# Optimization experiments

Hardware: AMD Instinct MI355X
Metric: run time of the kernel (lower is better)

Reference implementation:

```python
import jax, jax.numpy as jnp
import numpy as np

V = 50257      # vocab size
H = 512        # hidden size
S = 128        # source length
BEAM = 5       # beam width (matches beam_width=5 default)
TMAX = 32      # MAX_LENGTH decode cap
SOS, EOS = 1, 2
NEG = -1e9


def setup_inputs() -> dict:
    key = jax.random.key(0)
    ks = jax.random.split(key, 12)
    p = lambda k, shape: jax.random.normal(k, shape, jnp.float32) * 0.02
    return {
        "input_tokens": jax.random.randint(ks[0], (S,), 0, V),
        "embedding": p(ks[1], (V, H)),
        "enc_Wih": p(ks[2], (3 * H, H)),
        "enc_Whh": p(ks[3], (3 * H, H)),
        "enc_bih": jnp.zeros((3 * H,), jnp.float32),
        "enc_bhh": jnp.zeros((3 * H,), jnp.float32),
        "dec_Wih": p(ks[4], (3 * H, H)),
        "dec_Whh": p(ks[5], (3 * H, H)),
        "dec_bih": jnp.zeros((3 * H,), jnp.float32),
        "dec_bhh": jnp.zeros((3 * H,), jnp.float32),
        "W_concat": p(ks[6], (2 * H, H)),
        "W_vocab": p(ks[7], (H, V)),
    }


def gru_cell(x, h, Wih, Whh, bih, bhh):
    # x, h: [..., H]
    gi = x @ Wih.T + bih
    gh = h @ Whh.T + bhh
    ir, iz, inn = jnp.split(gi, 3, -1)
    hr, hz, hn = jnp.split(gh, 3, -1)
    r = jax.nn.sigmoid(ir + hr)
    z = jax.nn.sigmoid(iz + hz)
    n = jnp.tanh(inn + r * hn)
    return (1.0 - z) * n + z * h


def reference(input_tokens, embedding, enc_Wih, enc_Whh, enc_bih, enc_bhh,
              dec_Wih, dec_Whh, dec_bih, dec_bhh, W_concat, W_vocab):
    # ---- encoder: 1-layer GRU over source tokens ----
    src_emb = embedding[input_tokens]                       # [S, H]

    def enc_step(h, x):
        h2 = gru_cell(x, h, enc_Wih, enc_Whh, enc_bih, enc_bhh)
        return h2, h2

    enc_h, enc_out = jax.lax.scan(enc_step, jnp.zeros((H,), src_emb.dtype), src_emb)
    # enc_out: [S, H], enc_h: [H]

    def decode_step(tokens, hidden):
        # tokens: [B] int, hidden: [B, H]
        x = embedding[tokens]                               # [B, H]
        h = gru_cell(x, hidden, dec_Wih, dec_Whh, dec_bih, dec_bhh)
        attn = jax.nn.softmax(h @ enc_out.T, axis=-1)       # [B, S] Luong dot attention
        ctx = attn @ enc_out                                # [B, H]
        o = jnp.tanh(jnp.concatenate([h, ctx], -1) @ W_concat)
        logp = jax.nn.log_softmax(o @ W_vocab, axis=-1)     # [B, V]
        return logp, h

    # ---- batched beam search (GPU-resident equivalent of the heapq loop) ----
    tokens0 = jnp.full((BEAM,), SOS, jnp.int32)
    hidden0 = jnp.tile(enc_h[None], (BEAM, 1))
    scores0 = jnp.full((BEAM,), NEG, jnp.float32).at[0].set(0.0)
    fin0 = jnp.zeros((BEAM,), bool)
    len0 = jnp.ones((BEAM,), jnp.int32)
    seqs0 = jnp.zeros((BEAM, TMAX), jnp.int32)
    fin_row = jnp.full((V,), NEG, jnp.float32).at[EOS].set(0.0)

    def beam_step(state, t):
        tokens, hidden, scores, finished, lengths, seqs = state
        logp, h2 = decode_step(tokens, hidden)              # [BEAM, V]
        step_lp = jnp.where(finished[:, None], fin_row[None, :], logp)
        cand = scores[:, None] + step_lp                    # [BEAM, V]
        top_scores, flat = jax.lax.top_k(cand.reshape(-1), BEAM)
        parent = flat // V
        tok = (flat % V).astype(jnp.int32)
        par_fin = finished[parent]
        new_fin = par_fin | (tok == EOS)
        new_len = lengths[parent] + jnp.where(par_fin, 0, 1)
        new_seqs = seqs[parent].at[:, t].set(jnp.where(par_fin, 0, tok))
        return (tok, h2[parent], top_scores, new_fin, new_len, new_seqs), None

    state, _ = jax.lax.scan(beam_step, (tokens0, hidden0, scores0, fin0, len0, seqs0),
                            jnp.arange(TMAX))
    _, _, scores, _, lengths, seqs = state
    # length-normalized ranking, matching node.logp / node.leng sort
    norm = scores / lengths.astype(scores.dtype)
    order = jnp.argsort(-norm)
    return seqs[order], norm[order]
```

## Files before the change

### kernel.cpp

```cpp
#include <hip/hip_runtime.h>
#include <cstdint>
#include <cstddef>

#define V_SZ 50257
#define H_SZ 512
#define S_SZ 128
#define NBEAM 5
#define TMAXX 32
#define TOK_SOS 1
#define TOK_EOS 2
#define NEGINF (-1e9f)

#define GW 128
#define NT 512
#define GENC 16
#define COLS_PER_WG 393

#define VPAD 51200
#define CW4  400
#define WVP_OFF 1048576
#define WS_NEED (4194304ull + (size_t)H_SZ*VPAD*4ull)

#define BI_LEAF(l)  ((l)*32)
#define BI_ROOT     544
#define BI_REL(l)   (1024 + (l)*32)
#define BI_ECNT     1792
#define BI_EREL     1824

#define OF_GI    0
#define OF_ENC   196608
#define OF_EW    262144
#define OF_H2    327680
#define OF_AL    332800
#define OF_OTOP  333440
#define OF_PV    336000
#define OF_PM    342400
#define OF_PS    343680
#define OF_SC    344960
#define OI_BASE  344968
#define I_TOK 6400
#define I_FIN 6408
#define I_LEN 6416
#define I_PAR 6424
#define I_SEQ 6432

template <typename T>
__device__ __forceinline__ T aload(const T* p){
  return __hip_atomic_load((T*)p, __ATOMIC_RELAXED, __HIP_MEMORY_SCOPE_AGENT);
}
template <typename T>
__device__ __forceinline__ void astore(T* p, T v){
  __hip_atomic_store(p, v, __ATOMIC_RELAXED, __HIP_MEMORY_SCOPE_AGENT);
}

__device__ __forceinline__ float wredsum(float a){
#pragma unroll
  for (int m = 32; m; m >>= 1) a += __shfl_xor(a, m, 64);
  return a;
}

template <typename F>
__device__ __forceinline__ void dbar(int* bi, int wid, F&& tail){
  __shared__ int s_last;
  int mygen = 0;
  __syncthreads();
  if (threadIdx.x == 0){
    int leaf = wid >> 4;
    mygen = aload(bi + BI_REL(leaf));
    __builtin_amdgcn_s_waitcnt(0);
    int lo = __hip_atomic_fetch_add(bi + BI_LEAF(leaf), 1, __ATOMIC_RELAXED, __HIP_MEMORY_SCOPE_AGENT);
    int last = 0;
    if (lo == 15){
      astore(bi + BI_LEAF(leaf), 0);
      __builtin_amdgcn_s_waitcnt(0);
      int ro = __hip_atomic_fetch_add(bi + BI_ROOT, 1, __ATOMIC_RELAXED, __HIP_MEMORY_SCOPE_AGENT);
      if (ro == (GW/16) - 1){
        astore(bi + BI_ROOT, 0);
        last = 1;
      }
    }
    if (!last){
      while (aload(bi + BI_REL(leaf)) == mygen) __builtin_amdgcn_s_sleep(4);
    }
    s_last = last;
  }
  __syncthreads();
  if (s_last){
    tail();
    __syncthreads();
    if (threadIdx.x == 0){
      __builtin_amdgcn_s_waitcnt(0);
#pragma unroll
      for (int l = 0; l < GW/16; ++l) astore(bi + BI_REL(l), mygen + 1);
    }
  }
  __syncthreads();
}

__global__ __launch_bounds__(256)
void k_pack(const float* __restrict__ Wv, float* __restrict__ ws)
{
  float* wvp = ws + WVP_OFF;
  const int h  = blockIdx.y;
  const int v4 = blockIdx.x*256 + threadIdx.x;
  const int v  = v4*4;
  const float* src = Wv + (size_t)h*V_SZ;
  float4 o;
  o.x = (v+0 < V_SZ) ? src[v+0] : 0.f;
  o.y = (v+1 < V_SZ) ? src[v+1] : 0.f;
  o.z = (v+2 < V_SZ) ? src[v+2] : 0.f;
  o.w = (v+3 < V_SZ) ? src[v+3] : 0.f;
  *(float4*)(wvp + (size_t)h*VPAD + v) = o;
}

__global__ __launch_bounds__(256)
void k_gi(const int* __restrict__ toks, const float* __restrict__ emb,
          const float* __restrict__ eWih, const float* __restrict__ ebih,
          float* __restrict__ ws)
{
  float* fb = ws + 2048;
  float* gi = fb + OF_GI;
  const int tid = threadIdx.x, wid = blockIdx.x, lane = tid & 63, wvi = tid >> 6;
  int Wg = wid*4 + wvi;
  for (int it = 0; it < 192; ++it){
    int idx = Wg*192 + it;
    int s = idx / 1536, j = idx - s*1536;
    const float* er = emb + (size_t)toks[s]*H_SZ;
    const float* wr = eWih + (size_t)j*H_SZ;
    float a = 0.f;
#pragma unroll
    for (int u = 0; u < 8; ++u) a += er[u*64+lane]*wr[u*64+lane];
    a = wredsum(a);
    if (lane == 0) gi[idx] = a + ebih[j];
  }
  if (wid == 0){
    float* sc = fb + OF_SC;
    int* ib = (int*)(fb + OI_BASE);
    if (tid < NBEAM){
      sc[tid] = (tid==0) ? 0.f : NEGINF;
      ib[I_TOK+tid] = TOK_SOS; ib[I_FIN+tid] = 0; ib[I_LEN+tid] = 1; ib[I_PAR+tid] = 0;
    }
    for (int q = tid; q < 2*NBEAM*TMAXX; q += 256) ib[I_SEQ+q] = 0;
  }
}

__global__ __launch_bounds__(NT, 1)
void k_enc(const float* __restrict__ eWhh, const float* __restrict__ ebhh,
           float* __restrict__ ws)
{
  int* bi = (int*)ws;
  float* fb = ws + 2048;
  float* gi = fb + OF_GI;
  float* enc = fb + OF_ENC;
  const int tid = threadIdx.x, wid = blockIdx.x, lane = tid & 63, wvi = tid >> 6;
  const int i0 = wid*32;
  __shared__ float smF[96];

  float wreg[12][8];
#pragma unroll
  for (int dd = 0; dd < 12; ++dd){
    int d = wvi*12 + dd, g = d >> 5, il = d & 31;
    const float* wr = eWhh + (size_t)(g*512 + i0 + il)*H_SZ;
#pragma unroll
    for (int u = 0; u < 8; ++u) wreg[dd][u] = wr[u*64+lane];
  }
  float eb0 = 0.f, eb1 = 0.f, eb2 = 0.f;
  if (tid < 32){
    int i = i0 + tid;
    eb0 = ebhh[i]; eb1 = ebhh[512+i]; eb2 = ebhh[1024+i];
  }

  for (int s = 0; s < S_SZ; ++s){
    float hreg[8];
    if (s == 0){
#pragma unroll
      for (int u = 0; u < 8; ++u) hreg[u] = 0.f;
    } else {
      const float* hp = enc + (size_t)(s-1)*H_SZ;
#pragma unroll
      for (int u = 0; u < 8; ++u) hreg[u] = aload(hp + u*64 + lane);
    }
#pragma unroll
    for (int dd = 0; dd < 12; ++dd){
      float a = 0.f;
#pragma unroll
      for (int u = 0; u < 8; ++u) a += wreg[dd][u]*hreg[u];
      a = wredsum(a);
      if (lane == 0) smF[wvi*12 + dd] = a;
    }
    __syncthreads();
    if (tid < 32){
      int i = i0 + tid;
      float gr = smF[tid], gz = smF[32+tid], gn = smF[64+tid];
      float gir = gi[s*1536 + i], giz = gi[s*1536 + 512 + i], gin = gi[s*1536 + 1024 + i];
      float hprev = (s==0) ? 0.f : aload(enc + (s-1)*H_SZ + i);
      float r = 1.f/(1.f + expf(-(gir + gr + eb0)));
      float z = 1.f/(1.f + expf(-(giz + gz + eb1)));
      float n = tanhf(gin + r*(gn + eb2));
      astore(enc + s*H_SZ + i, (1.f - z)*n + z*hprev);
    }
    __syncthreads();
    if (tid == 0){
      int g = aload(bi + BI_EREL);
      __builtin_amdgcn_s_waitcnt(0);
      int lo = __hip_atomic_fetch_add(bi + BI_ECNT, 1, __ATOMIC_RELAXED, __HIP_MEMORY_SCOPE_AGENT);
      if (lo == GENC - 1){
        astore(bi + BI_ECNT, 0);
        __builtin_amdgcn_s_waitcnt(0);
        astore(bi + BI_EREL, g + 1);
      } else {
        while (aload(bi + BI_EREL) == g) __builtin_amdgcn_s_sleep(2);
      }
    }
    __syncthreads();
  }
}

__global__ __launch_bounds__(NT)
void k_ew(const float* __restrict__ Wc, float* __restrict__ ws)
{
  float* fb = ws + 2048;
  float* enc = fb + OF_ENC;
  float* EW  = fb + OF_EW;
  const int tid = threadIdx.x, wid = blockIdx.x;
  int jc = wid & 15, sb = wid >> 4;
  int jl = tid & 31, sl = (tid >> 5) & 15;
  int s = sb*16 + sl, j = jc*32 + jl;
  const float* er = enc + (size_t)s*H_SZ;
  const float* wc = Wc + (size_t)512*H_SZ;
  float a = 0.f;
  for (int k = 0; k < 512; ++k) a += er[k]*wc[(size_t)k*H_SZ + j];
  EW[s*H_SZ + j] = a;
}

template<int PACKED>
__global__ __launch_bounds__(NT, 1)
void k_dec(const float* __restrict__ emb,
           const float* __restrict__ dWih, const float* __restrict__ dWhh,
           const float* __restrict__ dbih, const float* __restrict__ dbhh,
           const float* __restrict__ Wc,  const float* __restrict__ Wv,
           float* __restrict__ out, float* __restrict__ ws)
{
  const int wid = blockIdx.x, tid = threadIdx.x;
  const int lane = tid & 63, wvi = tid >> 6;
  int* bi = (int*)ws;
  float* fb = ws + 2048;
  float* enc  = fb + OF_ENC;
  float* EW   = fb + OF_EW;
  float* h2   = fb + OF_H2;
  float* al   = fb + OF_AL;
  float* otop = fb + OF_OTOP;
  float* pv   = fb + OF_PV;
  float* pm   = fb + OF_PM;
  float* ps   = fb + OF_PS;
  float* sc   = fb + OF_SC;
  int* ib   = (int*)(fb + OI_BASE);
  int* pidx = ib;
  int* tokA = ib + I_TOK;
  int* finA = ib + I_FIN;
  int* lenA = ib + I_LEN;
  int* parA = ib + I_PAR;
  int* seqA = ib + I_SEQ;

  __shared__ float smF[512];
  __shared__ int   smI[256];
  __shared__ float s_buf[2560];
  __shared__ float s_pp[648];
  __shared__ float s_red[PACKED ? 6300 : 4];

  const int i0 = wid*4;

  for (int t = 0; t < TMAXX; ++t){
    float* h2new = h2 + (t & 1)*2560;
    float* h2old = h2 + ((t & 1) ^ 1)*2560;

    if (tid < NBEAM){ smI[tid] = aload(tokA + tid); smI[8 + tid] = t ? aload(parA + tid) : 0; }
    __syncthreads();
    if (t == 0){
      for (int q = tid; q < 2560; q += NT) s_buf[q] = enc[127*H_SZ + (q & 511)];
    } else {
      for (int q = tid; q < 2560; q += NT){
        int b = q >> 9;
        s_buf[q] = aload(h2old + smI[8 + b]*H_SZ + (q & 511));
      }
    }
    __syncthreads();
    {
      int mat = wvi >> 2;
      float srg[5][8];
      if (mat == 0){
#pragma unroll
        for (int b = 0; b < NBEAM; ++b){
          const float* sp = emb + (size_t)smI[b]*H_SZ;
#pragma unroll
          for (int u = 0; u < 8; ++u) srg[b][u] = sp[u*64+lane];
        }
      } else {
#pragma unroll
        for (int b = 0; b < NBEAM; ++b)
#pragma unroll
          for (int u = 0; u < 8; ++u) srg[b][u] = s_buf[b*512 + u*64 + lane];
      }
      for (int rr = 0; rr < 3; ++rr){
        int R = wvi*3 + rr;
        int rem = R - mat*12;
        int g = rem >> 2, il = rem & 3;
        const float* wr = ((mat==0) ? dWih : dWhh) + (size_t)(g*512 + i0 + il)*H_SZ;
        float wreg[8];
#pragma unroll
        for (int u = 0; u < 8; ++u) wreg[u] = wr[u*64+lane];
#pragma unroll
        for (int b = 0; b < NBEAM; ++b){
          float a = 0.f;
#pragma unroll
          for (int u = 0; u < 8; ++u) a += wreg[u]*srg[b][u];
          a = wredsum(a);
          if (lane == 0) smF[R*5 + b] = a;
        }
      }
      __syncthreads();
      if (tid < 20){
        int b = tid >> 2, il = tid & 3;
        int i = i0 + il;
        float ir  = smF[(0*12 + 0*4 + il)*5 + b] + dbih[i];
        float iz  = smF[(0*12 + 1*4 + il)*5 + b] + dbih[512+i];
        float inn = smF[(0*12 + 2*4 + il)*5 + b] + dbih[1024+i];
        float hr  = smF[(1*12 + 0*4 + il)*5 + b] + dbhh[i];
        float hz  = smF[(1*12 + 1*4 + il)*5 + b] + dbhh[512+i];
        float hn  = smF[(1*12 + 2*4 + il)*5 + b] + dbhh[1024+i];
        float r = 1.f/(1.f + expf(-(ir + hr)));
        float z = 1.f/(1.f + expf(-(iz + hz)));
        float n = tanhf(inn + r*hn);
        float hp = s_buf[b*512 + i];
        astore(h2new + b*H_SZ + i, (1.f - z)*n + z*hp);
      }
    }
    dbar(bi, wid, [&](){});

    for (int q = tid; q < 2560; q += NT) s_buf[q] = aload(h2new + q);
    __syncthreads();
    if (wvi < NBEAM){
      const float* er = enc + (size_t)wid*H_SZ;
      float a = 0.f;
#pragma unroll
      for (int u = 0; u < 8; ++u) a += er[u*64+lane]*s_buf[wvi*512 + u*64 + lane];
      a = wredsum(a);
      if (lane == 0) astore(al + wvi*S_SZ + wid, a);
    }
    if (tid < 320){
      int q = tid % 20, ksl = tid / 20;
      int f = wid*20 + q;
      int b = f >> 9, j = f & 511;
      float a = 0.f;
#pragma unroll 8
      for (int u = 0; u < 32; ++u){
        int k = ksl*32 + u;
        a += s_buf[b*512 + k]*Wc[(size_t)k*H_SZ + j];
      }
      smF[q*16 + ksl] = a;
    }
    __syncthreads();
    if (tid < 20){
      float a = 0.f;
#pragma unroll
      for (int u = 0; u < 16; ++u) a += smF[tid*16 + u];
      astore(otop + wid*20 + tid, a);
    }
    dbar(bi, wid, [&](){});

    if (wvi < NBEAM){
      float a1 = aload(al + wvi*S_SZ + lane), a2 = aload(al + wvi*S_SZ + 64 + lane);
      float m = fmaxf(a1, a2);
#pragma unroll
      for (int mm = 32; mm; mm >>= 1) m = fmaxf(m, __shfl_xor(m, mm, 64));
      float e1 = expf(a1 - m), e2 = expf(a2 - m);
      s_pp[wvi*128 + lane] = e1; s_pp[wvi*128 + 64 + lane] = e2;
      float ssv = wredsum(e1 + e2);
      if (lane == 0) s_pp[640 + wvi] = ssv;
    }
    __syncthreads();
    {
      float acc[5] = {0.f,0.f,0.f,0.f,0.f};
      for (int s2 = 0; s2 < 128; ++s2){
        float e = EW[(size_t)s2*H_SZ + tid];
#pragma unroll
        for (int b = 0; b < NBEAM; ++b) acc[b] += e*s_pp[b*128 + s2];
      }
#pragma unroll
      for (int b = 0; b < NBEAM; ++b)
        s_buf[b*512 + tid] = tanhf(aload(otop + b*512 + tid) + acc[b]/s_pp[640 + b]);
    }
    __syncthreads();

    if constexpr (PACKED){
      const float* wvp = (const float*)(ws + WVP_OFF);
      const int c4 = tid % 100, slice = tid / 100;
      float acc[5][4];
#pragma unroll
      for (int b = 0; b < 5; ++b)
#pragma unroll
        for (int k = 0; k < 4; ++k) acc[b][k] = 0.f;
      if (tid < 400){
        const float* wp = wvp + (size_t)(slice*128)*VPAD + wid*CW4 + c4*4;
        const int hbase = slice*128;
        float4 bufA[8], bufB[8];
#pragma unroll
        for (int u = 0; u < 8; ++u) bufA[u] = *(const float4*)(wp + (size_t)u*VPAD);
        for (int hb = 0; hb < 128; hb += 16){
#pragma unroll
          for (int u = 0; u < 8; ++u) bufB[u] = *(const float4*)(wp + (size_t)(hb+8+u)*VPAD);
#pragma unroll
          for (int u = 0; u < 8; ++u){
            float4 w = bufA[u]; int h = hbase + hb + u;
#pragma unroll
            for (int b = 0; b < 5; ++b){
              float o = s_buf[b*512 + h];
              acc[b][0] += w.x*o; acc[b][1] += w.y*o; acc[b][2] += w.z*o; acc[b][3] += w.w*o;
            }
          }
          if (hb + 16 < 128){
#pragma unroll
            for (int u = 0; u < 8; ++u) bufA[u] = *(const float4*)(wp + (size_t)(hb+16+u)*VPAD);
          }
#pragma unroll
          for (int u = 0; u < 8; ++u){
            float4 w = bufB[u]; int h = hbase + hb + 8 + u;
#pragma unroll
            for (int b = 0; b < 5; ++b){
              float o = s_buf[b*512 + h];
              acc[b][0] += w.x*o; acc[b][1] += w.y*o; acc[b][2] += w.z*o; acc[b][3] += w.w*o;
            }
          }
        }
      }
      if (tid < 400 && slice > 0){
        float* rp = s_red + (slice-1)*2100 + c4*21;
#pragma unroll
        for (int b = 0; b < 5; ++b)
#pragma unroll
          for (int k = 0; k < 4; ++k) rp[b*4+k] = acc[b][k];
      }
      __syncthreads();
      if (wvi < 2){
        if (tid < 100){
#pragma unroll
          for (int s = 0; s < 3; ++s){
            const float* rp = s_red + s*2100 + tid*21;
#pragma unroll
            for (int b = 0; b < 5; ++b)
#pragma unroll
              for (int k = 0; k < 4; ++k) acc[b][k] += rp[b*4+k];
          }
        }
        int vb4 = wid*CW4 + tid*4;
        bool okk[4];
#pragma unroll
        for (int k = 0; k < 4; ++k) okk[k] = (tid < 100) && (vb4 + k < V_SZ);
#pragma unroll
        for (int b = 0; b < NBEAM; ++b){
          float x[4]; int id[4];
#pragma unroll
          for (int k = 0; k < 4; ++k){
            x[k]  = okk[k] ? acc[b][k] : -3e38f;
            id[k] = okk[k] ? vb4 + k   : 0x7FFFFFFF;
          }
          float m = fmaxf(fmaxf(x[0],x[1]), fmaxf(x[2],x[3]));
#pragma unroll
          for (int mm = 32; mm; mm >>= 1) m = fmaxf(m, __shfl_xor(m, mm, 64));
          float e = 0.f;
#pragma unroll
          for (int k = 0; k < 4; ++k) e += expf(x[k] - m);
          float ssum = wredsum(e);
          float w5[5]; int i5[5];
#pragma unroll
          for (int r = 0; r < 5; ++r){
            float bv = x[0]; int bix = id[0];
#pragma unroll
            for (int k = 1; k < 4; ++k){
              bool take = (x[k] > bv) || (x[k] == bv && id[k] < bix);
              bv = take ? x[k] : bv; bix = take ? id[k] : bix;
            }
#pragma unroll
            for (int mm = 32; mm; mm >>= 1){
              float ov = __shfl_xor(bv, mm, 64); int oi = __shfl_xor(bix, mm, 64);
              bool take = (ov > bv) || (ov == bv && oi < bix);
              bv = take ? ov : bv; bix = take ? oi : bix;
            }
            w5[r] = bv; i5[r] = bix;
#pragma unroll
            for (int k = 0; k < 4; ++k)
              if (id[k] == bix){ x[k] = -3e38f; id[k] = 0x7FFFFFFF; }
          }
          if (lane == 0){
#pragma unroll
            for (int r = 0; r < 5; ++r){ smF[(wvi*5+b)*5+r] = w5[r]; smI[(wvi*5+b)*5+r] = i5[r]; }
            smF[300 + wvi*5 + b] = m;
            smF[360 + wvi*5 + b] = ssum;
          }
        }
      }
      __syncthreads();
      if (tid < NBEAM){
        float M = -3.4e38f, Sv = 0.f;
#pragma unroll
        for (int w8 = 0; w8 < 2; ++w8){
          float m2 = smF[300 + w8*5 + tid], s2 = smF[360 + w8*5 + tid];
          if (m2 > M){ Sv = Sv*expf(M - m2) + s2; M = m2; }
          else       { Sv = Sv + s2*expf(m2 - M); }
        }
        astore(pm + wid*5 + tid, M); astore(ps + wid*5 + tid, Sv);
      }
      if (wvi < NBEAM){
        int b = wvi;
        float cval; int cidx;
        if (lane < 10){ cval = smF[((lane/5)*5 + b)*5 + (lane%5)]; cidx = smI[((lane/5)*5 + b)*5 + (lane%5)]; }
        else { cval = -3e38f; cidx = 0x7FFFFFFF; }
        float bv = cval; int bc = cidx;
#pragma unroll
        for (int r = 0; r < 5; ++r){
          float cv2 = bv; int ci2 = bc;
#pragma unroll
          for (int mm = 32; mm; mm >>= 1){
            float ov = __shfl_xor(cv2, mm, 64); int oi = __shfl_xor(ci2, mm, 64);
            bool take = (ov > cv2) || (ov == cv2 && oi < ci2);
            cv2 = take ? ov : cv2; ci2 = take ? oi : ci2;
          }
          if (lane == 0){ astore(pv + (wid*5+b)*5+r, cv2); astore(pidx + (wid*5+b)*5+r, ci2); }
          if (bc == ci2) bv = -3e38f;
        }
      }
    } else {
      int vbase = wid*COLS_PER_WG;
      int v = vbase + tid;
      bool act = (tid < COLS_PER_WG) && (v < V_SZ);
      int vc = act ? v : vbase;
      const float* wp = Wv + vc;
      float a0=0.f,a1=0.f,a2=0.f,a3=0.f,a4=0.f;
      for (int hb = 0; hb < H_SZ; hb += 16){
        float wr[16];
#pragma unroll
        for (int u = 0; u < 16; ++u) wr[u] = wp[(size_t)(hb+u)*V_SZ];
#pragma unroll
        for (int u = 0; u < 16; ++u){
          float w = wr[u];
          a0 += w*s_buf[hb+u];
          a1 += w*s_buf[512+hb+u];
          a2 += w*s_buf[1024+hb+u];
          a3 += w*s_buf[1536+hb+u];
          a4 += w*s_buf[2048+hb+u];
        }
      }
      if (!act){ a0=a1=a2=a3=a4=-3e38f; }
      int myv = act ? v : 0x7FFFFFFF;
      float accs[5] = {a0,a1,a2,a3,a4};
#pragma unroll
      for (int b = 0; b < NBEAM; ++b){
        float x = accs[b];
        float m = x;
#pragma unroll
        for (int mm = 32; mm; mm >>= 1) m = fmaxf(m, __shfl_xor(m, mm, 64));
        float e = expf(x - m);
        float ssum = wredsum(e);
        float bv = x; int bc = myv;
        float w5[5]; int i5[5];
#pragma unroll
        for (int r = 0; r < 5; ++r){
          float cv2 = bv; int ci2 = bc;
#pragma unroll
          for (int mm = 32; mm; mm >>= 1){
            float ov = __shfl_xor(cv2, mm, 64); int oi = __shfl_xor(ci2, mm, 64);
            bool take = (ov > cv2) || (ov == cv2 && oi < ci2);
            cv2 = take ? ov : cv2; ci2 = take ? oi : ci2;
          }
          w5[r] = cv2; i5[r] = ci2;
          if (bc == ci2) bv = -3e38f;
        }
        if (lane == 0){
#pragma unroll
          for (int r = 0; r < 5; ++r){ smF[(wvi*5+b)*5+r] = w5[r]; smI[(wvi*5+b)*5+r] = i5[r]; }
          smF[300 + wvi*5 + b] = m;
          smF[360 + wvi*5 + b] = ssum;
        }
      }
      __syncthreads();
      if (tid < NBEAM){
        float M = -3.4e38f, Sv = 0.f;
#pragma unroll
        for (int w8 = 0; w8 < 8; ++w8){
          float m2 = smF[300 + w8*5 + tid], s2 = smF[360 + w8*5 + tid];
          if (m2 > M){ Sv = Sv*expf(M - m2) + s2; M = m2; }
          else       { Sv = Sv + s2*expf(m2 - M); }
        }
        astore(pm + wid*5 + tid, M); astore(ps + wid*5 + tid, Sv);
      }
      if (wvi < NBEAM){
        int b = wvi;
        float cval; int cidx;
        if (lane < 40){ cval = smF[((lane/5)*5 + b)*5 + (lane%5)]; cidx = smI[((lane/5)*5 + b)*5 + (lane%5)]; }
        else { cval = -3e38f; cidx = 0x7FFFFFFF; }
        float bv = cval; int bc = cidx;
#pragma unroll
        for (int r = 0; r < 5; ++r){
          float cv2 = bv; int ci2 = bc;
#pragma unroll
          for (int mm = 32; mm; mm >>= 1){
            float ov = __shfl_xor(cv2, mm, 64); int oi = __shfl_xor(ci2, mm, 64);
            bool take = (ov > cv2) || (ov == cv2 && oi < ci2);
            cv2 = take ? ov : cv2; ci2 = take ? oi : ci2;
          }
          if (lane == 0){ astore(pv + (wid*5+b)*5+r, cv2); astore(pidx + (wid*5+b)*5+r, ci2); }
          if (bc == ci2) bv = -3e38f;
        }
      }
    }

    dbar(bi, wid, [&](){
      int b5 = wvi;
      if (b5 < NBEAM){
        float m1 = aload(pm + lane*5 + b5), s1 = aload(ps + lane*5 + b5);
        float m2 = aload(pm + (64+lane)*5 + b5), s2 = aload(ps + (64+lane)*5 + b5);
        float M, Sv;
        if (m1 >= m2){ M = m1; Sv = s1 + s2*expf(m2 - m1); }
        else         { M = m2; Sv = s2 + s1*expf(m1 - m2); }
#pragma unroll
        for (int mm = 32; mm; mm >>= 1){
          float om = __shfl_xor(M, mm, 64), os = __shfl_xor(Sv, mm, 64);
          if (om > M){ Sv = Sv*expf(M - om) + os; M = om; }
          else       { Sv = Sv + os*expf(om - M); }
        }
        if (lane == 0){ smF[8 + b5] = M; smF[80 + b5] = logf(Sv); }
        float lv[5]; int li[5];
        float nv5[5]; int ni5[5];
#pragma unroll
        for (int r = 0; r < 5; ++r){
          lv[r]  = aload(pv + (lane*5 + b5)*5 + r);      li[r]  = aload(pidx + (lane*5 + b5)*5 + r);
          nv5[r] = aload(pv + ((64+lane)*5 + b5)*5 + r); ni5[r] = aload(pidx + ((64+lane)*5 + b5)*5 + r);
        }
        for (int r = 0; r < 5; ++r){
          bool ins = (nv5[r] > lv[4]) || (nv5[r] == lv[4] && ni5[r] < li[4]);
          if (!ins) break;
          lv[4] = nv5[r]; li[4] = ni5[r];
#pragma unroll
          for (int p = 4; p > 0; --p){
            bool sw = (lv[p] > lv[p-1]) || (lv[p] == lv[p-1] && li[p] < li[p-1]);
            if (sw){ float tv = lv[p]; lv[p] = lv[p-1]; lv[p-1] = tv;
                     int ti = li[p]; li[p] = li[p-1]; li[p-1] = ti; }
          }
        }
        float cv = lv[0]; int ci = li[0];
#pragma unroll
        for (int r = 0; r < 5; ++r){
          float xv = cv; int xi = ci;
#pragma unroll
          for (int mm = 32; mm; mm >>= 1){
            float ov = __shfl_xor(xv, mm, 64); int oi = __shfl_xor(xi, mm, 64);
            bool take = (ov > xv) || (ov == xv && oi < xi);
            xv = take ? ov : xv; xi = take ? oi : xi;
          }
          if (lane == 0){ smF[16 + b5*5 + r] = xv; smI[16 + b5*5 + r] = xi; }
          if (ci == xi){
            lv[0]=lv[1]; li[0]=li[1]; lv[1]=lv[2]; li[1]=li[2];
            lv[2]=lv[3]; li[2]=li[3]; lv[3]=lv[4]; li[3]=li[4];
            lv[4] = -3e38f; li[4] = 0x7FFFFFFF;
            cv = lv[0]; ci = li[0];
          }
        }
      }
      __syncthreads();
      if (wvi == 0){
        float cval = -3e38f; int cflat = 0x7FFFFFFF;
        int b = lane/5, k = lane - b*5;
        if (lane < 25){
          if (aload(finA + b)){
            if (k == 0){ cval = aload(sc + b) + 0.0f; cflat = b*V_SZ + TOK_EOS; }
          } else {
            cval = ((smF[16 + b*5 + k] - smF[8 + b]) - smF[80 + b]) + aload(sc + b);
            cflat = b*V_SZ + smI[16 + b*5 + k];
          }
        }
        float bv = cval; int bc = cflat;
#pragma unroll
        for (int r = 0; r < 5; ++r){
          float xv = bv; int xi = bc;
#pragma unroll
          for (int mm = 32; mm; mm >>= 1){
            float ov = __shfl_xor(xv, mm, 64); int oi = __shfl_xor(xi, mm, 64);
            bool take = (ov > xv) || (ov == xv && oi < xi);
            xv = take ? ov : xv; xi = take ? oi : xi;
          }
          if (lane == 0){ smF[48 + r] = xv; smI[48 + r] = xi; }
          if (bc == xi) bv = -3e38f;
        }
        if (lane < NBEAM){
          int r = lane;
          float nscore = smF[48 + r]; int nfl = smI[48 + r];
          int par = nfl / V_SZ; int tok = nfl - par*V_SZ;
          int ofin = aload(finA + par); int olen = aload(lenA + par);
          int nf = (ofin || tok == TOK_EOS) ? 1 : 0;
          int nl = olen + (ofin ? 0 : 1);
          astore(sc + r, nscore); astore(tokA + r, tok); astore(finA + r, nf);
          astore(lenA + r, nl); astore(parA + r, par);
          smI[56 + r] = par; smI[64 + r] = tok; smI[72 + r] = ofin; smI[80 + r] = nl;
          smF[56 + r] = nscore;
        }
      }
      __syncthreads();
      int cur = t & 1, nxt = 1 - cur;
      if (tid < 160){
        int r = tid >> 5, u = tid & 31;
        int par = smI[56 + r];
        int val = aload(seqA + cur*160 + par*32 + u);
        if (u == t) val = smI[72 + r] ? 0 : smI[64 + r];
        astore(seqA + nxt*160 + r*32 + u, val);
      }
      if (t == TMAXX - 1){
        __syncthreads();
        if (tid == 0){
          float nn[5];
#pragma unroll
          for (int r = 0; r < 5; ++r) nn[r] = smF[56 + r] / (float)smI[80 + r];
          int used = 0;
#pragma unroll
          for (int r = 0; r < 5; ++r){
            int best = -1;
            for (int q2 = 0; q2 < 5; ++q2){
              if (used & (1 << q2)) continue;
              if (best < 0 || nn[q2] > nn[best]) best = q2;
            }
            used |= (1 << best);
            smI[88 + r] = best; smF[64 + r] = nn[best];
          }
        }
        __syncthreads();
        if (tid < 160){
          int r = tid >> 5, u = tid & 31;
          int src = smI[88 + r];
          out[tid] = (float)aload(seqA + nxt*160 + src*32 + u);
        }
        if (tid >= 160 && tid < 165) out[tid] = smF[64 + (tid - 160)];
      }
    });
  }
}

extern "C" void kernel_launch(void* const* d_in, const int* in_sizes, int n_in,
                              void* d_out, int out_size, void* d_ws, size_t ws_size,
                              hipStream_t stream)
{
  (void)in_sizes; (void)n_in; (void)out_size;
  hipMemsetAsync(d_ws, 0, 8192, stream);
  float* ws = (float*)d_ws;
  const bool packed = ws_size >= (size_t)WS_NEED;
  if (packed){
    k_pack<<<dim3(50, 512), dim3(256), 0, stream>>>((const float*)d_in[11], ws);
  }
  k_gi<<<dim3(256), dim3(256), 0, stream>>>(
      (const int*)d_in[0], (const float*)d_in[1],
      (const float*)d_in[2], (const float*)d_in[4], ws);
  k_enc<<<dim3(GENC), dim3(NT), 0, stream>>>(
      (const float*)d_in[3], (const float*)d_in[5], ws);
  k_ew<<<dim3(128), dim3(NT), 0, stream>>>(
      (const float*)d_in[10], ws);
  if (packed){
    k_dec<1><<<dim3(GW), dim3(NT), 0, stream>>>(
        (const float*)d_in[1],
        (const float*)d_in[6], (const float*)d_in[7],
        (const float*)d_in[8], (const float*)d_in[9],
        (const float*)d_in[10], (const float*)d_in[11],
        (float*)d_out, ws);
  } else {
    k_dec<0><<<dim3(GW), dim3(NT), 0, stream>>>(
        (const float*)d_in[1],
        (const float*)d_in[6], (const float*)d_in[7],
        (const float*)d_in[8], (const float*)d_in[9],
        (const float*)d_in[10], (const float*)d_in[11],
        (float*)d_out, ws);
  }
}
```

Before: 4.329 ms.

## Store vocab projection weights in fp16 with residual-based top-k rescoring

The packed vocab weight is now stored as fp16, halving the bytes streamed each decode step in the dominant output-projection GEMV, which reuses the unpacked per-column loop structure. To recover accuracy, the pack kernel also writes a transposed fp16 residual (w minus fp16(w)). Each workgroup takes its top-8 candidates per beam, adds the residual dot product for those candidates, and re-sorts to pick the top-5. The log-sum-exp normaliser is still computed from the fp16-approximated logits, so scores carry small precision error, and the pack kernel is now a tiled transpose.

```diff
diff --git a/kernel.cpp b/kernel.cpp
--- a/kernel.cpp
+++ b/kernel.cpp
@@ -16,10 +16,10 @@
 #define GENC 16
 #define COLS_PER_WG 393
 
-#define VPAD 51200
-#define CW4  400
+#define VPAD2 50304
 #define WVP_OFF 1048576
-#define WS_NEED (4194304ull + (size_t)H_SZ*VPAD*4ull)
+#define WRT_OFF 13926400
+#define WS_NEED (4194304ull + 2ull*(size_t)H_SZ*VPAD2*2ull)
 
 #define BI_LEAF(l)  ((l)*32)
 #define BI_ROOT     544
@@ -100,17 +100,33 @@
 __global__ __launch_bounds__(256)
 void k_pack(const float* __restrict__ Wv, float* __restrict__ ws)
 {
-  float* wvp = ws + WVP_OFF;
-  const int h  = blockIdx.y;
-  const int v4 = blockIdx.x*256 + threadIdx.x;
-  const int v  = v4*4;
-  const float* src = Wv + (size_t)h*V_SZ;
-  float4 o;
-  o.x = (v+0 < V_SZ) ? src[v+0] : 0.f;
-  o.y = (v+1 < V_SZ) ? src[v+1] : 0.f;
-  o.z = (v+2 < V_SZ) ? src[v+2] : 0.f;
-  o.w = (v+3 < V_SZ) ? src[v+3] : 0.f;
-  *(float4*)(wvp + (size_t)h*VPAD + v) = o;
+  __shared__ float tile[64][65];
+  _Float16* wvh = (_Float16*)(ws + WVP_OFF);
+  _Float16* wrt = (_Float16*)(ws + WRT_OFF);
+  const int tid = threadIdx.x;
+  const int vt = blockIdx.x * 64;
+  const int ht = blockIdx.y * 64;
+  const int lv = tid & 63, rg = tid >> 6;
+#pragma unroll
+  for (int q = 0; q < 16; ++q){
+    int hh = rg*16 + q;
+    int v = vt + lv;
+    float w = (v < V_SZ) ? Wv[(size_t)(ht+hh)*V_SZ + v] : 0.f;
+    tile[hh][lv] = w;
+  }
+  __syncthreads();
+#pragma unroll
+  for (int q = 0; q < 16; ++q){
+    int hh = rg*16 + q;
+    wvh[(size_t)(ht+hh)*VPAD2 + vt + lv] = (_Float16)tile[hh][lv];
+  }
+#pragma unroll
+  for (int q = 0; q < 16; ++q){
+    int vv = rg*16 + q;
+    float w = tile[lv][vv];
+    float w16 = (float)(_Float16)w;
+    wrt[(size_t)(vt+vv)*H_SZ + ht + lv] = (_Float16)(w - w16);
+  }
 }
 
 __global__ __launch_bounds__(256)
@@ -266,7 +282,6 @@
   __shared__ int   smI[256];
   __shared__ float s_buf[2560];
   __shared__ float s_pp[648];
-  __shared__ float s_red[PACKED ? 6300 : 4];
 
   const int i0 = wid*4;
 
@@ -391,163 +406,43 @@
         s_buf[b*512 + tid] = tanhf(aload(otop + b*512 + tid) + acc[b]/s_pp[640 + b]);
     }
     __syncthreads();
-
-    if constexpr (PACKED){
-      const float* wvp = (const float*)(ws + WVP_OFF);
-      const int c4 = tid % 100, slice = tid / 100;
-      float acc[5][4];
-#pragma unroll
-      for (int b = 0; b < 5; ++b)
-#pragma unroll
-        for (int k = 0; k < 4; ++k) acc[b][k] = 0.f;
-      if (tid < 400){
-        const float* wp = wvp + (size_t)(slice*128)*VPAD + wid*CW4 + c4*4;
-        const int hbase = slice*128;
-        float4 bufA[8], bufB[8];
-#pragma unroll
-        for (int u = 0; u < 8; ++u) bufA[u] = *(const float4*)(wp + (size_t)u*VPAD);
-        for (int hb = 0; hb < 128; hb += 16){
-#pragma unroll
-          for (int u = 0; u < 8; ++u) bufB[u] = *(const float4*)(wp + (size_t)(hb+8+u)*VPAD);
-#pragma unroll
-          for (int u = 0; u < 8; ++u){
-            float4 w = bufA[u]; int h = hbase + hb + u;
-#pragma unroll
-            for (int b = 0; b < 5; ++b){
-              float o = s_buf[b*512 + h];
-              acc[b][0] += w.x*o; acc[b][1] += w.y*o; acc[b][2] += w.z*o; acc[b][3] += w.w*o;
-            }
-          }
-          if (hb + 16 < 128){
-#pragma unroll
-            for (int u = 0; u < 8; ++u) bufA[u] = *(const float4*)(wp + (size_t)(hb+16+u)*VPAD);
-          }
-#pragma unroll
-          for (int u = 0; u < 8; ++u){
-            float4 w = bufB[u]; int h = hbase + hb + 8 + u;
-#pragma unroll
-            for (int b = 0; b < 5; ++b){
-              float o = s_buf[b*512 + h];
-              acc[b][0] += w.x*o; acc[b][1] += w.y*o; acc[b][2] += w.z*o; acc[b][3] += w.w*o;
-            }
-          }
-        }
-      }
-      if (tid < 400 && slice > 0){
-        float* rp = s_red + (slice-1)*2100 + c4*21;
-#pragma unroll
-        for (int b = 0; b < 5; ++b)
-#pragma unroll
-          for (int k = 0; k < 4; ++k) rp[b*4+k] = acc[b][k];
-      }
-      __syncthreads();
-      if (wvi < 2){
-        if (tid < 100){
-#pragma unroll
-          for (int s = 0; s < 3; ++s){
-            const float* rp = s_red + s*2100 + tid*21;
-#pragma unroll
-            for (int b = 0; b < 5; ++b)
-#pragma unroll
-              for (int k = 0; k < 4; ++k) acc[b][k] += rp[b*4+k];
-          }
-        }
-        int vb4 = wid*CW4 + tid*4;
-        bool okk[4];
-#pragma unroll
-        for (int k = 0; k < 4; ++k) okk[k] = (tid < 100) && (vb4 + k < V_SZ);
-#pragma unroll
-        for (int b = 0; b < NBEAM; ++b){
-          float x[4]; int id[4];
-#pragma unroll
-          for (int k = 0; k < 4; ++k){
-            x[k]  = okk[k] ? acc[b][k] : -3e38f;
-            id[k] = okk[k] ? vb4 + k   : 0x7FFFFFFF;
-          }
-          float m = fmaxf(fmaxf(x[0],x[1]), fmaxf(x[2],x[3]));
-#pragma unroll
-          for (int mm = 32; mm; mm >>= 1) m = fmaxf(m, __shfl_xor(m, mm, 64));
-          float e = 0.f;
-#pragma unroll
-          for (int k = 0; k < 4; ++k) e += expf(x[k] - m);
-          float ssum = wredsum(e);
-          float w5[5]; int i5[5];
-#pragma unroll
-          for (int r = 0; r < 5; ++r){
-            float bv = x[0]; int bix = id[0];
-#pragma unroll
-            for (int k = 1; k < 4; ++k){
-              bool take = (x[k] > bv) || (x[k] == bv && id[k] < bix);
-              bv = take ? x[k] : bv; bix = take ? id[k] : bix;
-            }
-#pragma unroll
-            for (int mm = 32; mm; mm >>= 1){
-              float ov = __shfl_xor(bv, mm, 64); int oi = __shfl_xor(bix, mm, 64);
-              bool take = (ov > bv) || (ov == bv && oi < bix);
-              bv = take ? ov : bv; bix = take ? oi : bix;
-            }
-            w5[r] = bv; i5[r] = bix;
-#pragma unroll
-            for (int k = 0; k < 4; ++k)
-              if (id[k] == bix){ x[k] = -3e38f; id[k] = 0x7FFFFFFF; }
-          }
-          if (lane == 0){
-#pragma unroll
-            for (int r = 0; r < 5; ++r){ smF[(wvi*5+b)*5+r] = w5[r]; smI[(wvi*5+b)*5+r] = i5[r]; }
-            smF[300 + wvi*5 + b] = m;
-            smF[360 + wvi*5 + b] = ssum;
-          }
-        }
-      }
-      __syncthreads();
-      if (tid < NBEAM){
-        float M = -3.4e38f, Sv = 0.f;
-#pragma unroll
-        for (int w8 = 0; w8 < 2; ++w8){
-          float m2 = smF[300 + w8*5 + tid], s2 = smF[360 + w8*5 + tid];
-          if (m2 > M){ Sv = Sv*expf(M - m2) + s2; M = m2; }
-          else       { Sv = Sv + s2*expf(m2 - M); }
-        }
-        astore(pm + wid*5 + tid, M); astore(ps + wid*5 + tid, Sv);
-      }
-      if (wvi < NBEAM){
-        int b = wvi;
-        float cval; int cidx;
-        if (lane < 10){ cval = smF[((lane/5)*5 + b)*5 + (lane%5)]; cidx = smI[((lane/5)*5 + b)*5 + (lane%5)]; }
-        else { cval = -3e38f; cidx = 0x7FFFFFFF; }
-        float bv = cval; int bc = cidx;
-#pragma unroll
-        for (int r = 0; r < 5; ++r){
-          float cv2 = bv; int ci2 = bc;
-#pragma unroll
-          for (int mm = 32; mm; mm >>= 1){
-            float ov = __shfl_xor(cv2, mm, 64); int oi = __shfl_xor(ci2, mm, 64);
-            bool take = (ov > cv2) || (ov == cv2 && oi < ci2);
-            cv2 = take ? ov : cv2; ci2 = take ? oi : ci2;
-          }
-          if (lane == 0){ astore(pv + (wid*5+b)*5+r, cv2); astore(pidx + (wid*5+b)*5+r, ci2); }
-          if (bc == ci2) bv = -3e38f;
-        }
-      }
-    } else {
+    {
       int vbase = wid*COLS_PER_WG;
       int v = vbase + tid;
       bool act = (tid < COLS_PER_WG) && (v < V_SZ);
       int vc = act ? v : vbase;
-      const float* wp = Wv + vc;
       float a0=0.f,a1=0.f,a2=0.f,a3=0.f,a4=0.f;
-      for (int hb = 0; hb < H_SZ; hb += 16){
-        float wr[16];
-#pragma unroll
-        for (int u = 0; u < 16; ++u) wr[u] = wp[(size_t)(hb+u)*V_SZ];
-#pragma unroll
-        for (int u = 0; u < 16; ++u){
-          float w = wr[u];
-          a0 += w*s_buf[hb+u];
-          a1 += w*s_buf[512+hb+u];
-          a2 += w*s_buf[1024+hb+u];
-          a3 += w*s_buf[1536+hb+u];
-          a4 += w*s_buf[2048+hb+u];
+      if constexpr (PACKED){
+        const _Float16* wp = (const _Float16*)(ws + WVP_OFF) + vc;
+        for (int hb = 0; hb < H_SZ; hb += 16){
+          float wr[16];
+#pragma unroll
+          for (int u = 0; u < 16; ++u) wr[u] = (float)wp[(size_t)(hb+u)*VPAD2];
+#pragma unroll
+          for (int u = 0; u < 16; ++u){
+            float w = wr[u];
+            a0 += w*s_buf[hb+u];
+            a1 += w*s_buf[512+hb+u];
+            a2 += w*s_buf[1024+hb+u];
+            a3 += w*s_buf[1536+hb+u];
+            a4 += w*s_buf[2048+hb+u];
+          }
+        }
+      } else {
+        const float* wp = Wv + vc;
+        for (int hb = 0; hb < H_SZ; hb += 16){
+          float wr[16];
+#pragma unroll
+          for (int u = 0; u < 16; ++u) wr[u] = wp[(size_t)(hb+u)*V_SZ];
+#pragma unroll
+          for (int u = 0; u < 16; ++u){
+            float w = wr[u];
+            a0 += w*s_buf[hb+u];
+            a1 += w*s_buf[512+hb+u];
+            a2 += w*s_buf[1024+hb+u];
+            a3 += w*s_buf[1536+hb+u];
+            a4 += w*s_buf[2048+hb+u];
+          }
         }
       }
       if (!act){ a0=a1=a2=a3=a4=-3e38f; }
@@ -593,23 +488,83 @@
         }
         astore(pm + wid*5 + tid, M); astore(ps + wid*5 + tid, Sv);
       }
-      if (wvi < NBEAM){
-        int b = wvi;
-        float cval; int cidx;
-        if (lane < 40){ cval = smF[((lane/5)*5 + b)*5 + (lane%5)]; cidx = smI[((lane/5)*5 + b)*5 + (lane%5)]; }
-        else { cval = -3e38f; cidx = 0x7FFFFFFF; }
-        float bv = cval; int bc = cidx;
-#pragma unroll
-        for (int r = 0; r < 5; ++r){
-          float cv2 = bv; int ci2 = bc;
-#pragma unroll
-          for (int mm = 32; mm; mm >>= 1){
-            float ov = __shfl_xor(cv2, mm, 64); int oi = __shfl_xor(ci2, mm, 64);
-            bool take = (ov > cv2) || (ov == cv2 && oi < ci2);
-            cv2 = take ? ov : cv2; ci2 = take ? oi : ci2;
-          }
-          if (lane == 0){ astore(pv + (wid*5+b)*5+r, cv2); astore(pidx + (wid*5+b)*5+r, ci2); }
-          if (bc == ci2) bv = -3e38f;
+
+      if constexpr (PACKED){
+        if (wvi < NBEAM){
+          int b = wvi;
+          float cval; int cidx;
+          if (lane < 40){ cval = smF[((lane/5)*5 + b)*5 + (lane%5)]; cidx = smI[((lane/5)*5 + b)*5 + (lane%5)]; }
+          else { cval = -3e38f; cidx = 0x7FFFFFFF; }
+          float bv = cval; int bc = cidx;
+#pragma unroll
+          for (int r = 0; r < 8; ++r){
+            float cv2 = bv; int ci2 = bc;
+#pragma unroll
+            for (int mm = 32; mm; mm >>= 1){
+              float ov = __shfl_xor(cv2, mm, 64); int oi = __shfl_xor(ci2, mm, 64);
+              bool take = (ov > cv2) || (ov == cv2 && oi < ci2);
+              cv2 = take ? ov : cv2; ci2 = take ? oi : ci2;
+            }
+            if (lane == 0){ smF[400 + b*8 + r] = cv2; smI[200 + b*8 + r] = ci2; }
+            if (bc == ci2) bv = -3e38f;
+          }
+        }
+        __syncthreads();
+        {
+          const _Float16* wrt = (const _Float16*)(ws + WRT_OFF);
+          for (int pp = 0; pp < 5; ++pp){
+            int p = wvi*5 + pp;
+            int b = p >> 3, k = p & 7;
+            int idx = smI[200 + b*8 + k];
+            bool valid = (idx != 0x7FFFFFFF);
+            int ic = valid ? idx : 0;
+            const _Float16* rr = wrt + (size_t)ic*H_SZ + lane*8;
+            const float* ob = s_buf + b*512 + lane*8;
+            float d = 0.f;
+#pragma unroll
+            for (int u = 0; u < 8; ++u) d += (float)rr[u]*ob[u];
+            d = wredsum(d);
+            if (lane == 0 && valid) smF[400 + b*8 + k] += d;
+          }
+        }
+        __syncthreads();
+        if (tid < NBEAM){
+          float v8[8]; int i8[8];
+#pragma unroll
+          for (int k = 0; k < 8; ++k){ v8[k] = smF[400 + tid*8 + k]; i8[k] = smI[200 + tid*8 + k]; }
+#pragma unroll
+          for (int a = 1; a < 8; ++a){
+            float vv = v8[a]; int ii = i8[a];
+            int p = a;
+            while (p > 0 && ((v8[p-1] < vv) || (v8[p-1] == vv && i8[p-1] > ii))){
+              v8[p] = v8[p-1]; i8[p] = i8[p-1]; --p;
+            }
+            v8[p] = vv; i8[p] = ii;
+          }
+#pragma unroll
+          for (int r = 0; r < 5; ++r){
+            astore(pv + (wid*5+tid)*5+r, v8[r]); astore(pidx + (wid*5+tid)*5+r, i8[r]);
+          }
+        }
+      } else {
+        if (wvi < NBEAM){
+          int b = wvi;
+          float cval; int cidx;
+          if (lane < 40){ cval = smF[((lane/5)*5 + b)*5 + (lane%5)]; cidx = smI[((lane/5)*5 + b)*5 + (lane%5)]; }
+          else { cval = -3e38f; cidx = 0x7FFFFFFF; }
+          float bv = cval; int bc = cidx;
+#pragma unroll
+          for (int r = 0; r < 5; ++r){
+            float cv2 = bv; int ci2 = bc;
+#pragma unroll
+            for (int mm = 32; mm; mm >>= 1){
+              float ov = __shfl_xor(cv2, mm, 64); int oi = __shfl_xor(ci2, mm, 64);
+              bool take = (ov > cv2) || (ov == cv2 && oi < ci2);
+              cv2 = take ? ov : cv2; ci2 = take ? oi : ci2;
+            }
+            if (lane == 0){ astore(pv + (wid*5+b)*5+r, cv2); astore(pidx + (wid*5+b)*5+r, ci2); }
+            if (bc == ci2) bv = -3e38f;
+          }
         }
       }
     }
@@ -752,7 +707,7 @@
   float* ws = (float*)d_ws;
   const bool packed = ws_size >= (size_t)WS_NEED;
   if (packed){
-    k_pack<<<dim3(50, 512), dim3(256), 0, stream>>>((const float*)d_in[11], ws);
+    k_pack<<<dim3(VPAD2/64, 8), dim3(256), 0, stream>>>((const float*)d_in[11], ws);
   }
   k_gi<<<dim3(256), dim3(256), 0, stream>>>(
       (const int*)d_in[0], (const float*)d_in[1],
```

Measured after the change: 4.004 ms. 7.5% less time.
